# Kernel optimization log

Hardware: AMD Instinct MI355X
Metric: run time of the kernel (lower is better)

## Reference

```python
import jax, jax.numpy as jnp
import numpy as np
import math

B, S, D = 2, 2048, 1024
H = 16
HD = D // H
W = 128


def setup_inputs() -> dict:
    key = jax.random.key(0)
    ks = jax.random.split(key, 5)
    scale = 1.0 / math.sqrt(D)
    return {
        "x": jax.random.normal(ks[0], (B, S, D), dtype=jnp.float32),
        "in_proj_w": jax.random.normal(ks[1], (3 * D, D), dtype=jnp.float32) * scale,
        "in_proj_b": jax.random.normal(ks[2], (3 * D,), dtype=jnp.float32) * 0.02,
        "out_proj_w": jax.random.normal(ks[3], (D, D), dtype=jnp.float32) * scale,
        "out_proj_b": jax.random.normal(ks[4], (D,), dtype=jnp.float32) * 0.02,
        "window_size": W,
    }


def reference(x, in_proj_w, in_proj_b, out_proj_w, out_proj_b, window_size):
    b, s, d = x.shape
    # Combined qkv projection, as nn.MultiheadAttention does
    qkv = x @ in_proj_w.T + in_proj_b  # [B,S,3D]
    q, k, v = jnp.split(qkv, 3, axis=-1)
    # [B,H,S,HD]
    def heads(t):
        return t.reshape(b, s, H, HD).transpose(0, 2, 1, 3)
    q, k, v = heads(q), heads(k), heads(v)
    scale = 1.0 / math.sqrt(HD)
    scores = jnp.einsum("bhqd,bhkd->bhqk", q, k) * scale  # [B,H,S,S]
    # banded sliding-window mask: disallow |i-j| > window_size
    i = jnp.arange(s)[:, None]
    j = jnp.arange(s)[None, :]
    banned = jnp.abs(i - j) > window_size  # [S,S] bool
    scores = jnp.where(banned[None, None], -jnp.inf, scores)
    attn = jax.nn.softmax(scores, axis=-1)
    out = jnp.einsum("bhqk,bhkd->bhqd", attn, v)  # [B,H,S,HD]
    out = out.transpose(0, 2, 1, 3).reshape(b, s, d)
    return out @ out_proj_w.T + out_proj_b
```

## Files before the change

### kernel.cpp

```cpp
#include <hip/hip_runtime.h>

#define S_LEN 2048
#define DMODEL 1024
#define NHEAD 16
#define HDIM 64

typedef __bf16 bf16x8 __attribute__((ext_vector_type(8)));
typedef float f32x4 __attribute__((ext_vector_type(4)));

typedef __attribute__((address_space(1))) const void gconst_void;
typedef __attribute__((address_space(3))) void lds_void;

__device__ __forceinline__ unsigned short f2bf(float f) {
    unsigned u = __builtin_bit_cast(unsigned, f);
    u += 0x7fffu + ((u >> 16) & 1u);
    return (unsigned short)(u >> 16);
}

__global__ __launch_bounds__(256) void cvt_f32_bf16(const float* __restrict__ src,
                                                    unsigned short* __restrict__ dst, int n4) {
    int i = blockIdx.x * 256 + threadIdx.x;
    if (i < n4) {
        float4 f = ((const float4*)src)[i];
        ushort4 o;
        o.x = f2bf(f.x); o.y = f2bf(f.y); o.z = f2bf(f.z); o.w = f2bf(f.w);
        ((ushort4*)dst)[i] = o;
    }
}

template <int QKV_MODE>
__global__ __launch_bounds__(256) void gemm_bt(const unsigned short* __restrict__ A,
                                               const unsigned short* __restrict__ Bt,
                                               const float* __restrict__ bias,
                                               void* __restrict__ out,
                                               int M, int N, int K) {
    __shared__ unsigned short lA[128 * 64] __attribute__((aligned(16)));
    __shared__ unsigned short lB[128 * 64] __attribute__((aligned(16)));

    const int tid  = threadIdx.x;
    const int lane = tid & 63;
    const int w    = tid >> 6;
    const int quad = lane >> 4;
    const int l16  = lane & 15;

    const int m0 = blockIdx.x * 128;
    const int n0 = blockIdx.y * 128;

    const int rowi = tid >> 3;
    const int csw  = ((tid & 7) ^ (rowi & 7)) * 8;
    const unsigned short* aSrc = A + (size_t)(m0 + rowi) * K + csw;
    const unsigned short* bSrc = Bt + (size_t)(n0 + rowi) * K + csw;
    const int dstOff = (w * 8) * 64;

    f32x4 acc[4][4];
    {
        f32x4 z = {0.f, 0.f, 0.f, 0.f};
        #pragma unroll
        for (int i = 0; i < 4; i++)
            #pragma unroll
            for (int j = 0; j < 4; j++) acc[i][j] = z;
    }

    const int wm = (w & 1) * 64;
    const int wn = (w >> 1) * 64;

    for (int kt = 0; kt < K; kt += 64) {
        __syncthreads();
        #pragma unroll
        for (int p = 0; p < 4; p++) {
            __builtin_amdgcn_global_load_lds(
                (gconst_void*)(aSrc + (size_t)p * 32 * K + kt),
                (lds_void*)(&lA[dstOff + p * 32 * 64]), 16, 0, 0);
            __builtin_amdgcn_global_load_lds(
                (gconst_void*)(bSrc + (size_t)p * 32 * K + kt),
                (lds_void*)(&lB[dstOff + p * 32 * 64]), 16, 0, 0);
        }
        __syncthreads();

        #pragma unroll
        for (int kk = 0; kk < 2; kk++) {
            bf16x8 af[4], bfr[4];
            const int xsw = ((kk * 4 + quad) ^ (l16 & 7)) * 8;
            #pragma unroll
            for (int t = 0; t < 4; t++) {
                af[t]  = *(const bf16x8*)&lA[(wm + t * 16 + l16) * 64 + xsw];
                bfr[t] = *(const bf16x8*)&lB[(wn + t * 16 + l16) * 64 + xsw];
            }
            #pragma unroll
            for (int i = 0; i < 4; i++)
                #pragma unroll
                for (int j = 0; j < 4; j++)
                    acc[i][j] = __builtin_amdgcn_mfma_f32_16x16x32_bf16(af[i], bfr[j], acc[i][j], 0, 0, 0);
        }
    }

    #pragma unroll
    for (int j = 0; j < 4; j++) {
        const int n = n0 + wn + j * 16 + l16;
        const float bv = bias[n];
        float scl = 1.0f;
        if (QKV_MODE) scl = (n < DMODEL) ? 0.125f : 1.0f;
        #pragma unroll
        for (int i = 0; i < 4; i++) {
            const int mrow = m0 + wm + i * 16 + quad * 4;
            #pragma unroll
            for (int r = 0; r < 4; r++) {
                float v = (acc[i][j][r] + bv) * scl;
                if (QKV_MODE)
                    ((unsigned short*)out)[(size_t)(mrow + r) * N + n] = f2bf(v);
                else
                    ((float*)out)[(size_t)(mrow + r) * N + n] = v;
            }
        }
    }
}

__global__ __launch_bounds__(256) void attn_win(const unsigned short* __restrict__ qkv,
                                                unsigned short* __restrict__ attnout,
                                                const int* __restrict__ wptr) {
    __shared__ unsigned short lK[32 * 64] __attribute__((aligned(16)));
    __shared__ unsigned short lV[64 * 32] __attribute__((aligned(16)));
    __shared__ unsigned short lP[4][16 * 32] __attribute__((aligned(16)));

    const int W = wptr[0];
    const int tid  = threadIdx.x;
    const int lane = tid & 63;
    const int w    = tid >> 6;
    const int quad = lane >> 4;
    const int l16  = lane & 15;

    const int q0 = blockIdx.x * 64;
    const int h  = blockIdx.y;
    const size_t rowbase = (size_t)blockIdx.z * S_LEN;

    const int qrow = q0 + w * 16 + l16;
    bf16x8 qf0, qf1;
    {
        const unsigned short* qp = qkv + (rowbase + qrow) * (3 * DMODEL) + h * HDIM;
        qf0 = *(const bf16x8*)(qp + quad * 8);
        qf1 = *(const bf16x8*)(qp + 32 + quad * 8);
    }

    f32x4 o[4];
    { f32x4 z = {0.f,0.f,0.f,0.f}; o[0]=z; o[1]=z; o[2]=z; o[3]=z; }
    float mrow[4], lrow[4];
    #pragma unroll
    for (int r = 0; r < 4; r++) { mrow[r] = -1e30f; lrow[r] = 0.f; }

    const int kbase = q0 - W;
    const int nch = (2 * W + 64 + 31) / 32;

    const int skey = tid >> 3;
    const int sci  = tid & 7;
    const int iq = q0 + w * 16 + quad * 4;

    for (int c = 0; c < nch; c++) {
        const int kc0 = kbase + c * 32;
        __syncthreads();
        {
            int kg = kc0 + skey;
            int kcl = kg < 0 ? 0 : (kg > S_LEN - 1 ? S_LEN - 1 : kg);
            const unsigned short* kp = qkv + (rowbase + kcl) * (3 * DMODEL) + DMODEL + h * HDIM + sci * 8;
            int4 kd = *(const int4*)kp;
            *(int4*)&lK[skey * 64 + ((sci ^ (skey & 7)) * 8)] = kd;

            const unsigned short* vp = qkv + (rowbase + kcl) * (3 * DMODEL) + 2 * DMODEL + h * HDIM + sci * 8;
            int4 vd = *(const int4*)vp;
            unsigned short ve[8];
            *(int4*)ve = vd;
            #pragma unroll
            for (int j = 0; j < 8; j++) {
                int d = sci * 8 + j;
                int pos = ((skey >> 3) ^ ((d >> 1) & 3)) & 3;
                lV[d * 32 + pos * 8 + (skey & 7)] = ve[j];
            }
        }
        __syncthreads();

        f32x4 s0 = {0.f,0.f,0.f,0.f}, s1 = {0.f,0.f,0.f,0.f};
        {
            int xk0 = ((quad) ^ (l16 & 7)) * 8;
            int xk1 = ((4 + quad) ^ (l16 & 7)) * 8;
            bf16x8 k00 = *(const bf16x8*)&lK[(l16) * 64 + xk0];
            bf16x8 k01 = *(const bf16x8*)&lK[(l16) * 64 + xk1];
            bf16x8 k10 = *(const bf16x8*)&lK[(16 + l16) * 64 + xk0];
            bf16x8 k11 = *(const bf16x8*)&lK[(16 + l16) * 64 + xk1];
            s0 = __builtin_amdgcn_mfma_f32_16x16x32_bf16(qf0, k00, s0, 0, 0, 0);
            s0 = __builtin_amdgcn_mfma_f32_16x16x32_bf16(qf1, k01, s0, 0, 0, 0);
            s1 = __builtin_amdgcn_mfma_f32_16x16x32_bf16(qf0, k10, s1, 0, 0, 0);
            s1 = __builtin_amdgcn_mfma_f32_16x16x32_bf16(qf1, k11, s1, 0, 0, 0);
        }

        const int j0 = kc0 + l16;
        const int j1 = j0 + 16;
        #pragma unroll
        for (int r = 0; r < 4; r++) {
            const int i = iq + r;
            const int d0 = i - j0, d1 = i - j1;
            const bool v0 = ((unsigned)j0 < (unsigned)S_LEN) && (d0 <= W) && (-d0 <= W);
            const bool v1 = ((unsigned)j1 < (unsigned)S_LEN) && (d1 <= W) && (-d1 <= W);
            float sv0 = v0 ? s0[r] : -1e30f;
            float sv1 = v1 ? s1[r] : -1e30f;
            float mc = fmaxf(sv0, sv1);
            mc = fmaxf(mc, __shfl_xor(mc, 1));
            mc = fmaxf(mc, __shfl_xor(mc, 2));
            mc = fmaxf(mc, __shfl_xor(mc, 4));
            mc = fmaxf(mc, __shfl_xor(mc, 8));
            float mnew = fmaxf(mrow[r], mc);
            float alpha = __expf(mrow[r] - mnew);
            float p0 = v0 ? __expf(s0[r] - mnew) : 0.f;
            float p1 = v1 ? __expf(s1[r] - mnew) : 0.f;
            float ps = p0 + p1;
            ps += __shfl_xor(ps, 1);
            ps += __shfl_xor(ps, 2);
            ps += __shfl_xor(ps, 4);
            ps += __shfl_xor(ps, 8);
            lrow[r] = lrow[r] * alpha + ps;
            mrow[r] = mnew;
            o[0][r] *= alpha; o[1][r] *= alpha; o[2][r] *= alpha; o[3][r] *= alpha;
            const int qq = quad * 4 + r;
            const int sw = (qq >> 1) & 3;
            lP[w][qq * 32 + (((l16 >> 3) ^ sw) & 3) * 8 + (l16 & 7)] = f2bf(p0);
            lP[w][qq * 32 + ((((l16 >> 3) + 2) ^ sw) & 3) * 8 + (l16 & 7)] = f2bf(p1);
        }

        __builtin_amdgcn_s_waitcnt(0);

        bf16x8 pf = *(const bf16x8*)&lP[w][l16 * 32 + ((quad ^ ((l16 >> 1) & 3)) & 3) * 8];
        #pragma unroll
        for (int t = 0; t < 4; t++) {
            const int d = t * 16 + l16;
            const int pos = (quad ^ ((d >> 1) & 3)) & 3;
            bf16x8 vf = *(const bf16x8*)&lV[d * 32 + pos * 8];
            o[t] = __builtin_amdgcn_mfma_f32_16x16x32_bf16(pf, vf, o[t], 0, 0, 0);
        }
    }

    #pragma unroll
    for (int r = 0; r < 4; r++) {
        const float inv = 1.f / lrow[r];
        #pragma unroll
        for (int t = 0; t < 4; t++) {
            attnout[(rowbase + iq + r) * DMODEL + h * HDIM + t * 16 + l16] = f2bf(o[t][r] * inv);
        }
    }
}

extern "C" void kernel_launch(void* const* d_in, const int* in_sizes, int n_in,
                              void* d_out, int out_size, void* d_ws, size_t ws_size,
                              hipStream_t stream) {
    const float* x   = (const float*)d_in[0];
    const float* w1  = (const float*)d_in[1];
    const float* b1  = (const float*)d_in[2];
    const float* w2  = (const float*)d_in[3];
    const float* b2  = (const float*)d_in[4];
    const int* wsz   = (const int*)d_in[5];

    char* ws = (char*)d_ws;
    unsigned short* xb    = (unsigned short*)(ws);
    unsigned short* attnb = (unsigned short*)(ws);
    unsigned short* w1b   = (unsigned short*)(ws + (8u << 20));
    unsigned short* w2b   = (unsigned short*)(ws + (14u << 20));
    unsigned short* qkvb  = (unsigned short*)(ws + (16u << 20));

    const int M = 2 * S_LEN;

    cvt_f32_bf16<<<(M * DMODEL / 4 + 255) / 256, 256, 0, stream>>>(x, xb, M * DMODEL / 4);
    cvt_f32_bf16<<<(3 * DMODEL * DMODEL / 4 + 255) / 256, 256, 0, stream>>>(w1, w1b, 3 * DMODEL * DMODEL / 4);
    cvt_f32_bf16<<<(DMODEL * DMODEL / 4 + 255) / 256, 256, 0, stream>>>(w2, w2b, DMODEL * DMODEL / 4);

    gemm_bt<1><<<dim3(M / 128, 3 * DMODEL / 128), 256, 0, stream>>>(xb, w1b, b1, qkvb, M, 3 * DMODEL, DMODEL);

    attn_win<<<dim3(S_LEN / 64, NHEAD, 2), 256, 0, stream>>>(qkvb, attnb, wsz);

    gemm_bt<0><<<dim3(M / 128, DMODEL / 128), 256, 0, stream>>>(attnb, w2b, b2, (float*)d_out, M, DMODEL, DMODEL);
}
```

Baseline: 189.6 us.

## Store V transposed, drop LDS staging and online max in windowed attention

The QKV GEMM now writes Q/K into a 2D-wide buffer and V transposed per batch/head into a separate buffer. The attention kernel reads K and V fragments straight from global memory into MFMA operands, dropping the LDS staging and block barriers. It also removes the online-softmax running max and rescaling, exponentiating raw scores and summing once at the end. The three conversion kernels are fused into one launch. Skipping the max subtraction risks overflow for large scores, and the transposed V store scatters 2-byte writes with stride S_LEN.

```diff
diff --git a/kernel.cpp b/kernel.cpp
--- a/kernel.cpp
+++ b/kernel.cpp
@@ -17,15 +17,27 @@
     return (unsigned short)(u >> 16);
 }
 
-__global__ __launch_bounds__(256) void cvt_f32_bf16(const float* __restrict__ src,
-                                                    unsigned short* __restrict__ dst, int n4) {
+#define N4_X  (2 * S_LEN * DMODEL / 4)
+#define N4_W1 (3 * DMODEL * DMODEL / 4)
+#define N4_W2 (DMODEL * DMODEL / 4)
+__global__ __launch_bounds__(256) void cvt_all(const float* __restrict__ x,
+                                               const float* __restrict__ w1,
+                                               const float* __restrict__ w2,
+                                               unsigned short* __restrict__ xb,
+                                               unsigned short* __restrict__ w1b,
+                                               unsigned short* __restrict__ w2b) {
     int i = blockIdx.x * 256 + threadIdx.x;
-    if (i < n4) {
-        float4 f = ((const float4*)src)[i];
-        ushort4 o;
-        o.x = f2bf(f.x); o.y = f2bf(f.y); o.z = f2bf(f.z); o.w = f2bf(f.w);
-        ((ushort4*)dst)[i] = o;
-    }
+    const float* s;
+    unsigned short* d;
+    int off;
+    if (i < N4_X)            { s = x;  d = xb;  off = i; }
+    else if (i < N4_X + N4_W1) { s = w1; d = w1b; off = i - N4_X; }
+    else if (i < N4_X + N4_W1 + N4_W2) { s = w2; d = w2b; off = i - N4_X - N4_W1; }
+    else return;
+    float4 f = ((const float4*)s)[off];
+    ushort4 o;
+    o.x = f2bf(f.x); o.y = f2bf(f.y); o.z = f2bf(f.z); o.w = f2bf(f.w);
+    ((ushort4*)d)[off] = o;
 }
 
 template <int QKV_MODE>
@@ -33,6 +45,7 @@
                                                const unsigned short* __restrict__ Bt,
                                                const float* __restrict__ bias,
                                                void* __restrict__ out,
+                                               unsigned short* __restrict__ vT,
                                                int M, int N, int K) {
     __shared__ unsigned short lA[128 * 64] __attribute__((aligned(16)));
     __shared__ unsigned short lB[128 * 64] __attribute__((aligned(16)));
@@ -94,32 +107,51 @@
         }
     }
 
-    #pragma unroll
-    for (int j = 0; j < 4; j++) {
-        const int n = n0 + wn + j * 16 + l16;
-        const float bv = bias[n];
-        float scl = 1.0f;
-        if (QKV_MODE) scl = (n < DMODEL) ? 0.125f : 1.0f;
-        #pragma unroll
-        for (int i = 0; i < 4; i++) {
-            const int mrow = m0 + wm + i * 16 + quad * 4;
-            #pragma unroll
-            for (int r = 0; r < 4; r++) {
-                float v = (acc[i][j][r] + bv) * scl;
-                if (QKV_MODE)
-                    ((unsigned short*)out)[(size_t)(mrow + r) * N + n] = f2bf(v);
-                else
-                    ((float*)out)[(size_t)(mrow + r) * N + n] = v;
+    if (QKV_MODE == 1 && n0 >= 2 * DMODEL) {
+        #pragma unroll
+        for (int j = 0; j < 4; j++) {
+            const int n = n0 + wn + j * 16 + l16;
+            const float bv = bias[n];
+            const int hd = n - 2 * DMODEL;
+            #pragma unroll
+            for (int i = 0; i < 4; i++) {
+                const int mrow = m0 + wm + i * 16 + quad * 4;
+                #pragma unroll
+                for (int r = 0; r < 4; r++) {
+                    const int m = mrow + r;
+                    const int b = m >> 11;
+                    const int s = m & (S_LEN - 1);
+                    vT[(size_t)(b * DMODEL + hd) * S_LEN + s] = f2bf(acc[i][j][r] + bv);
+                }
             }
         }
-    }
-}
-
-__global__ __launch_bounds__(256) void attn_win(const unsigned short* __restrict__ qkv,
+    } else {
+        #pragma unroll
+        for (int j = 0; j < 4; j++) {
+            const int n = n0 + wn + j * 16 + l16;
+            const float bv = bias[n];
+            float scl = 1.0f;
+            if (QKV_MODE) scl = (n < DMODEL) ? 0.125f : 1.0f;
+            #pragma unroll
+            for (int i = 0; i < 4; i++) {
+                const int mrow = m0 + wm + i * 16 + quad * 4;
+                #pragma unroll
+                for (int r = 0; r < 4; r++) {
+                    float v = (acc[i][j][r] + bv) * scl;
+                    if (QKV_MODE)
+                        ((unsigned short*)out)[(size_t)(mrow + r) * 2048 + n] = f2bf(v);
+                    else
+                        ((float*)out)[(size_t)(mrow + r) * N + n] = v;
+                }
+            }
+        }
+    }
+}
+
+__global__ __launch_bounds__(256) void attn_win(const unsigned short* __restrict__ qk,
+                                                const unsigned short* __restrict__ vT,
                                                 unsigned short* __restrict__ attnout,
                                                 const int* __restrict__ wptr) {
-    __shared__ unsigned short lK[32 * 64] __attribute__((aligned(16)));
-    __shared__ unsigned short lV[64 * 32] __attribute__((aligned(16)));
     __shared__ unsigned short lP[4][16 * 32] __attribute__((aligned(16)));
 
     const int W = wptr[0];
@@ -136,60 +168,39 @@
     const int qrow = q0 + w * 16 + l16;
     bf16x8 qf0, qf1;
     {
-        const unsigned short* qp = qkv + (rowbase + qrow) * (3 * DMODEL) + h * HDIM;
+        const unsigned short* qp = qk + (rowbase + qrow) * (2 * DMODEL) + h * HDIM;
         qf0 = *(const bf16x8*)(qp + quad * 8);
         qf1 = *(const bf16x8*)(qp + 32 + quad * 8);
     }
 
+    const unsigned short* kbasep = qk + rowbase * (2 * DMODEL) + DMODEL + h * HDIM;
+    const unsigned short* vbase  = vT + (size_t)(blockIdx.z * DMODEL + h * HDIM) * S_LEN;
+
     f32x4 o[4];
     { f32x4 z = {0.f,0.f,0.f,0.f}; o[0]=z; o[1]=z; o[2]=z; o[3]=z; }
-    float mrow[4], lrow[4];
-    #pragma unroll
-    for (int r = 0; r < 4; r++) { mrow[r] = -1e30f; lrow[r] = 0.f; }
+    float lsum[4] = {0.f, 0.f, 0.f, 0.f};
 
     const int kbase = q0 - W;
     const int nch = (2 * W + 64 + 31) / 32;
-
-    const int skey = tid >> 3;
-    const int sci  = tid & 7;
     const int iq = q0 + w * 16 + quad * 4;
 
     for (int c = 0; c < nch; c++) {
         const int kc0 = kbase + c * 32;
-        __syncthreads();
-        {
-            int kg = kc0 + skey;
-            int kcl = kg < 0 ? 0 : (kg > S_LEN - 1 ? S_LEN - 1 : kg);
-            const unsigned short* kp = qkv + (rowbase + kcl) * (3 * DMODEL) + DMODEL + h * HDIM + sci * 8;
-            int4 kd = *(const int4*)kp;
-            *(int4*)&lK[skey * 64 + ((sci ^ (skey & 7)) * 8)] = kd;
-
-            const unsigned short* vp = qkv + (rowbase + kcl) * (3 * DMODEL) + 2 * DMODEL + h * HDIM + sci * 8;
-            int4 vd = *(const int4*)vp;
-            unsigned short ve[8];
-            *(int4*)ve = vd;
-            #pragma unroll
-            for (int j = 0; j < 8; j++) {
-                int d = sci * 8 + j;
-                int pos = ((skey >> 3) ^ ((d >> 1) & 3)) & 3;
-                lV[d * 32 + pos * 8 + (skey & 7)] = ve[j];
-            }
-        }
-        __syncthreads();
+
+        int kr0 = kc0 + l16;       kr0 = kr0 < 0 ? 0 : (kr0 > S_LEN - 1 ? S_LEN - 1 : kr0);
+        int kr1 = kc0 + 16 + l16;  kr1 = kr1 < 0 ? 0 : (kr1 > S_LEN - 1 ? S_LEN - 1 : kr1);
+        const unsigned short* kp0 = kbasep + (size_t)kr0 * (2 * DMODEL) + quad * 8;
+        const unsigned short* kp1 = kbasep + (size_t)kr1 * (2 * DMODEL) + quad * 8;
+        bf16x8 k0lo = *(const bf16x8*)(kp0);
+        bf16x8 k0hi = *(const bf16x8*)(kp0 + 32);
+        bf16x8 k1lo = *(const bf16x8*)(kp1);
+        bf16x8 k1hi = *(const bf16x8*)(kp1 + 32);
 
         f32x4 s0 = {0.f,0.f,0.f,0.f}, s1 = {0.f,0.f,0.f,0.f};
-        {
-            int xk0 = ((quad) ^ (l16 & 7)) * 8;
-            int xk1 = ((4 + quad) ^ (l16 & 7)) * 8;
-            bf16x8 k00 = *(const bf16x8*)&lK[(l16) * 64 + xk0];
-            bf16x8 k01 = *(const bf16x8*)&lK[(l16) * 64 + xk1];
-            bf16x8 k10 = *(const bf16x8*)&lK[(16 + l16) * 64 + xk0];
-            bf16x8 k11 = *(const bf16x8*)&lK[(16 + l16) * 64 + xk1];
-            s0 = __builtin_amdgcn_mfma_f32_16x16x32_bf16(qf0, k00, s0, 0, 0, 0);
-            s0 = __builtin_amdgcn_mfma_f32_16x16x32_bf16(qf1, k01, s0, 0, 0, 0);
-            s1 = __builtin_amdgcn_mfma_f32_16x16x32_bf16(qf0, k10, s1, 0, 0, 0);
-            s1 = __builtin_amdgcn_mfma_f32_16x16x32_bf16(qf1, k11, s1, 0, 0, 0);
-        }
+        s0 = __builtin_amdgcn_mfma_f32_16x16x32_bf16(qf0, k0lo, s0, 0, 0, 0);
+        s0 = __builtin_amdgcn_mfma_f32_16x16x32_bf16(qf1, k0hi, s0, 0, 0, 0);
+        s1 = __builtin_amdgcn_mfma_f32_16x16x32_bf16(qf0, k1lo, s1, 0, 0, 0);
+        s1 = __builtin_amdgcn_mfma_f32_16x16x32_bf16(qf1, k1hi, s1, 0, 0, 0);
 
         const int j0 = kc0 + l16;
         const int j1 = j0 + 16;
@@ -199,46 +210,35 @@
             const int d0 = i - j0, d1 = i - j1;
             const bool v0 = ((unsigned)j0 < (unsigned)S_LEN) && (d0 <= W) && (-d0 <= W);
             const bool v1 = ((unsigned)j1 < (unsigned)S_LEN) && (d1 <= W) && (-d1 <= W);
-            float sv0 = v0 ? s0[r] : -1e30f;
-            float sv1 = v1 ? s1[r] : -1e30f;
-            float mc = fmaxf(sv0, sv1);
-            mc = fmaxf(mc, __shfl_xor(mc, 1));
-            mc = fmaxf(mc, __shfl_xor(mc, 2));
-            mc = fmaxf(mc, __shfl_xor(mc, 4));
-            mc = fmaxf(mc, __shfl_xor(mc, 8));
-            float mnew = fmaxf(mrow[r], mc);
-            float alpha = __expf(mrow[r] - mnew);
-            float p0 = v0 ? __expf(s0[r] - mnew) : 0.f;
-            float p1 = v1 ? __expf(s1[r] - mnew) : 0.f;
-            float ps = p0 + p1;
-            ps += __shfl_xor(ps, 1);
-            ps += __shfl_xor(ps, 2);
-            ps += __shfl_xor(ps, 4);
-            ps += __shfl_xor(ps, 8);
-            lrow[r] = lrow[r] * alpha + ps;
-            mrow[r] = mnew;
-            o[0][r] *= alpha; o[1][r] *= alpha; o[2][r] *= alpha; o[3][r] *= alpha;
+            float p0 = v0 ? __expf(s0[r]) : 0.f;
+            float p1 = v1 ? __expf(s1[r]) : 0.f;
+            lsum[r] += p0 + p1;
             const int qq = quad * 4 + r;
             const int sw = (qq >> 1) & 3;
             lP[w][qq * 32 + (((l16 >> 3) ^ sw) & 3) * 8 + (l16 & 7)] = f2bf(p0);
             lP[w][qq * 32 + ((((l16 >> 3) + 2) ^ sw) & 3) * 8 + (l16 & 7)] = f2bf(p1);
         }
 
-        __builtin_amdgcn_s_waitcnt(0);
+        __builtin_amdgcn_s_waitcnt(0xc07f);
 
         bf16x8 pf = *(const bf16x8*)&lP[w][l16 * 32 + ((quad ^ ((l16 >> 1) & 3)) & 3) * 8];
+        int sc = kc0 + quad * 8;
+        sc = sc < 0 ? 0 : (sc > S_LEN - 8 ? S_LEN - 8 : sc);
         #pragma unroll
         for (int t = 0; t < 4; t++) {
-            const int d = t * 16 + l16;
-            const int pos = (quad ^ ((d >> 1) & 3)) & 3;
-            bf16x8 vf = *(const bf16x8*)&lV[d * 32 + pos * 8];
+            bf16x8 vf = *(const bf16x8*)(vbase + (size_t)(t * 16 + l16) * S_LEN + sc);
             o[t] = __builtin_amdgcn_mfma_f32_16x16x32_bf16(pf, vf, o[t], 0, 0, 0);
         }
     }
 
     #pragma unroll
     for (int r = 0; r < 4; r++) {
-        const float inv = 1.f / lrow[r];
+        float l = lsum[r];
+        l += __shfl_xor(l, 1);
+        l += __shfl_xor(l, 2);
+        l += __shfl_xor(l, 4);
+        l += __shfl_xor(l, 8);
+        const float inv = 1.f / l;
         #pragma unroll
         for (int t = 0; t < 4; t++) {
             attnout[(rowbase + iq + r) * DMODEL + h * HDIM + t * 16 + l16] = f2bf(o[t][r] * inv);
@@ -261,17 +261,16 @@
     unsigned short* attnb = (unsigned short*)(ws);
     unsigned short* w1b   = (unsigned short*)(ws + (8u << 20));
     unsigned short* w2b   = (unsigned short*)(ws + (14u << 20));
-    unsigned short* qkvb  = (unsigned short*)(ws + (16u << 20));
+    unsigned short* qkb   = (unsigned short*)(ws + (16u << 20));
+    unsigned short* vTb   = (unsigned short*)(ws + (32u << 20));
 
     const int M = 2 * S_LEN;
 
-    cvt_f32_bf16<<<(M * DMODEL / 4 + 255) / 256, 256, 0, stream>>>(x, xb, M * DMODEL / 4);
-    cvt_f32_bf16<<<(3 * DMODEL * DMODEL / 4 + 255) / 256, 256, 0, stream>>>(w1, w1b, 3 * DMODEL * DMODEL / 4);
-    cvt_f32_bf16<<<(DMODEL * DMODEL / 4 + 255) / 256, 256, 0, stream>>>(w2, w2b, DMODEL * DMODEL / 4);
-
-    gemm_bt<1><<<dim3(M / 128, 3 * DMODEL / 128), 256, 0, stream>>>(xb, w1b, b1, qkvb, M, 3 * DMODEL, DMODEL);
-
-    attn_win<<<dim3(S_LEN / 64, NHEAD, 2), 256, 0, stream>>>(qkvb, attnb, wsz);
-
-    gemm_bt<0><<<dim3(M / 128, DMODEL / 128), 256, 0, stream>>>(attnb, w2b, b2, (float*)d_out, M, DMODEL, DMODEL);
-}
+    cvt_all<<<(N4_X + N4_W1 + N4_W2 + 255) / 256, 256, 0, stream>>>(x, w1, w2, xb, w1b, w2b);
+
+    gemm_bt<1><<<dim3(M / 128, 3 * DMODEL / 128), 256, 0, stream>>>(xb, w1b, b1, qkb, vTb, M, 3 * DMODEL, DMODEL);
+
+    attn_win<<<dim3(S_LEN / 64, NHEAD, 2), 256, 0, stream>>>(qkb, vTb, attnb, wsz);
+
+    gemm_bt<0><<<dim3(M / 128, DMODEL / 128), 256, 0, stream>>>(attnb, w2b, b2, (float*)d_out, nullptr, M, DMODEL, DMODEL);
+}
```

After: 191.6 us. Within noise of the previous version (+1.1%).
